# Performance work log

Hardware: AMD Instinct MI355X
Metric: run time of the kernel (lower is better)

## Reference

```python
import jax, jax.numpy as jnp
import numpy as np

HEAD_DIM = 64
FEAT_DIM = 64
WINDOW = 64
EPS = 1e-6


def _performer_phi(x, proj):
    # x: [..., D] float32, proj: [F, D]  ->  [..., F]
    scaled = x / (HEAD_DIM ** 0.25)
    projected = jnp.einsum('...d,fd->...f', scaled, proj)
    sq_norm = 0.5 * jnp.sum(scaled * scaled, axis=-1, keepdims=True)
    logits = jnp.clip(projected - sq_norm, -20.0, 20.0)
    return jnp.exp(logits) / np.sqrt(float(FEAT_DIM))


def setup_inputs() -> dict:
    key = jax.random.key(0)
    kq, kk, kv, kp = jax.random.split(key, 4)
    B, H, Hkv, T, D = 2, 32, 8, 4096, HEAD_DIM
    q = jax.random.normal(kq, (B, H, T, D), dtype=jnp.float32)
    k = jax.random.normal(kk, (B, Hkv, T, D), dtype=jnp.float32)
    v = jax.random.normal(kv, (B, Hkv, T, D), dtype=jnp.float32)
    # performer projection: orthogonal block, row-normalized (as in _build_projection_matrix)
    g = np.asarray(jax.random.normal(kp, (D, D), dtype=jnp.float32))
    qm, _ = np.linalg.qr(g)
    mat = qm[:, :FEAT_DIM].T  # [F, D]
    mat = mat / np.maximum(np.linalg.norm(mat, axis=-1, keepdims=True), 1e-6)
    proj = jnp.asarray(mat, dtype=jnp.float32)
    return {'q': q, 'k': k, 'v': v, 'proj': proj}


def reference(q, k, v, proj):
    # Hybrid attention: exact local-window softmax (current + previous block,
    # causal) fused with linear (Performer) attention over all fully-evicted
    # blocks via a recurrent SSD state, sharing a single normalizer.
    B, H, T, D = q.shape
    Hkv = k.shape[1]
    G = H // Hkv  # query heads per kv group (query_to_kv = arange(H) // G)
    W = WINDOW
    nb = T // W
    f32 = jnp.float32

    phi_q = _performer_phi(q.astype(f32), proj.astype(f32))  # [B,H,T,F]
    phi_k = _performer_phi(k.astype(f32), proj.astype(f32))  # [B,Hkv,T,F]

    pq = phi_q.reshape(B, Hkv, G, nb, W, FEAT_DIM)
    pk = phi_k.reshape(B, Hkv, nb, W, FEAT_DIM)
    qb = q.astype(f32).reshape(B, Hkv, G, nb, W, D)
    kb = k.astype(f32).reshape(B, Hkv, nb, W, D)
    vb = v.astype(f32).reshape(B, Hkv, nb, W, D)

    # ---- linear-attention recurrent state (state_decay = 1.0 -> plain cumsum)
    # state at query block c covers all blocks <= c-2 (blocks fully outside the
    # local window).
    S_blk = jnp.einsum('bknwf,bknwd->bknfd', pk, vb)  # [B,Hkv,nb,F,D]
    z_blk = pk.sum(axis=3)                            # [B,Hkv,nb,F]
    S_cum = jnp.cumsum(S_blk, axis=2)
    z_cum = jnp.cumsum(z_blk, axis=2)
    S_used = jnp.concatenate([jnp.zeros_like(S_cum[:, :, :2]), S_cum[:, :, :-2]], axis=2)
    z_used = jnp.concatenate([jnp.zeros_like(z_cum[:, :, :2]), z_cum[:, :, :-2]], axis=2)

    num_lin = jnp.einsum('bkgnwf,bknfd->bkgnwd', pq, S_used)  # [B,Hkv,G,nb,W,D]
    den_lin = jnp.einsum('bkgnwf,bknf->bkgnw', pq, z_used)    # [B,Hkv,G,nb,W]

    # ---- local softmax attention over [previous block | current block]
    k_prev = jnp.concatenate([jnp.zeros_like(kb[:, :, :1]), kb[:, :, :-1]], axis=2)
    v_prev = jnp.concatenate([jnp.zeros_like(vb[:, :, :1]), vb[:, :, :-1]], axis=2)
    kk2 = jnp.concatenate([k_prev, kb], axis=3)  # [B,Hkv,nb,2W,D]
    vv2 = jnp.concatenate([v_prev, vb], axis=3)

    scores = jnp.einsum('bkgnwd,bknxd->bkgnwx', qb, kk2) / np.sqrt(float(D))
    jj = jnp.arange(W)[:, None]        # query offset in block
    ii = jnp.arange(2 * W)[None, :]    # key offset in 2-block window
    causal = ii <= (W + jj)            # [W, 2W]
    has_prev = (jnp.arange(nb) > 0)[:, None, None]
    mask = causal[None] & (has_prev | (ii >= W)[None])  # [nb, W, 2W]
    a = jnp.where(mask[None, None, None], jnp.exp(jnp.clip(scores, -30.0, 30.0)), 0.0)

    num_loc = jnp.einsum('bkgnwx,bknxd->bkgnwd', a, vv2)
    den = a.sum(axis=-1) + den_lin + EPS  # shared normalizer

    out = (num_loc + num_lin) / den[..., None]
    return out.reshape(B, H, T, D).astype(q.dtype)
```

## Files before the change

### kernel.cpp

```cpp
#include <hip/hip_runtime.h>

#define BB 2
#define HKV 8
#define HH 32
#define TT 4096
#define NBLK 64
#define SCL 0.35355339059327373f
#define LOG2E 1.4426950408889634f

typedef __attribute__((ext_vector_type(8))) short short8;
typedef __attribute__((ext_vector_type(4))) float f32x4;
typedef unsigned int u32;

__device__ __forceinline__ unsigned short f2bf(float x) {
    union { float f; u32 u; } v; v.f = x;
    u32 r = v.u + 0x7fffu + ((v.u >> 16) & 1u);
    return (unsigned short)(r >> 16);
}
__device__ __forceinline__ u32 pk2(float lo, float hi) {
    u32 r;
    asm("v_cvt_pk_bf16_f32 %0, %1, %2" : "=v"(r) : "v"(lo), "v"(hi));
    return r;
}
__device__ __forceinline__ float bf2f(unsigned short b) {
    union { u32 u; float f; } v; v.u = ((u32)b) << 16; return v.f;
}
__device__ __forceinline__ f32x4 mfma16(short8 a, short8 b, f32x4 c) {
    return __builtin_amdgcn_mfma_f32_16x16x32_bf16(a, b, c, 0, 0, 0);
}
__device__ __forceinline__ short8 ldsfrag(const char* base, int row, int off) {
    int b = (row << 7) + off;
    b ^= (row & 7) << 4;
    return *(const short8*)(base + b);
}
__device__ __forceinline__ short8 xform(f32x4 t0, f32x4 t1, int lane) {
    const int c = lane & 15, g = lane >> 4;
    u32 p00 = pk2(t0[0], t0[1]), p01 = pk2(t0[2], t0[3]);
    u32 p10 = pk2(t1[0], t1[1]), p11 = pk2(t1[2], t1[3]);
    int srcA = c + 32 * (g & 1);
    int srcB = srcA + 16;
    u32 a00 = (u32)__shfl((int)p00, srcA);
    u32 a01 = (u32)__shfl((int)p01, srcA);
    u32 a10 = (u32)__shfl((int)p10, srcA);
    u32 a11 = (u32)__shfl((int)p11, srcA);
    u32 b00 = (u32)__shfl((int)p00, srcB);
    u32 b01 = (u32)__shfl((int)p01, srcB);
    u32 b10 = (u32)__shfl((int)p10, srcB);
    u32 b11 = (u32)__shfl((int)p11, srcB);
    bool hi = (g & 2);
    union { u32 u[4]; short8 s; } r;
    r.u[0] = hi ? a10 : a00;
    r.u[1] = hi ? a11 : a01;
    r.u[2] = hi ? b10 : b00;
    r.u[3] = hi ? b11 : b01;
    return r.s;
}
__device__ __forceinline__ void gld16(const void* g, void* l) {
    __builtin_amdgcn_global_load_lds((const __attribute__((address_space(1))) u32*)g,
                                     (__attribute__((address_space(3))) u32*)l, 16, 0, 0);
}

__global__ __launch_bounds__(256, 4) void k_phase1(
        const float* __restrict__ kg, const float* __restrict__ vg,
        const float* __restrict__ pg,
        char* __restrict__ sblk, char* __restrict__ kbf, char* __restrict__ vbf,
        float* __restrict__ zg) {
    __shared__ __align__(16) char kb_s[8192];
    __shared__ __align__(16) char vt_s[8192];
    __shared__ float sqn_s[64];

    const int tid = threadIdx.x;
    const int bid = blockIdx.x;
    const size_t base = (size_t)bid * 4096;

#pragma unroll
    for (int j = 0; j < 4; ++j) {
        int i4 = tid + j * 256;
        int key = i4 >> 4, d0 = (i4 & 15) << 2;
        float4 fk = *(const float4*)(kg + base + key * 64 + d0);
        float s0 = fk.x * SCL, s1 = fk.y * SCL, s2 = fk.z * SCL, s3 = fk.w * SCL;
        int byte = (key << 7) + (d0 << 1); byte ^= (key & 7) << 4;
        *(uint2*)(kb_s + byte) = make_uint2(pk2(s0, s1), pk2(s2, s3));
        float ps = 0.5f * (s0 * s0 + s1 * s1 + s2 * s2 + s3 * s3);
        ps += __shfl_xor(ps, 1);
        ps += __shfl_xor(ps, 2);
        ps += __shfl_xor(ps, 4);
        ps += __shfl_xor(ps, 8);
        if ((tid & 15) == 0) sqn_s[key] = ps;
    }
    {
        int d = tid & 63, kq = tid >> 6;
        const float* vp = vg + base + (size_t)kq * 16 * 64 + d;
        union { unsigned short h[16]; uint4 q[2]; } pk;
#pragma unroll
        for (int i = 0; i < 16; ++i) pk.h[i] = f2bf(vp[i * 64]);
        int b0 = ((d << 7) + (kq << 5)) ^ ((d & 7) << 4);
        int b1 = ((d << 7) + (kq << 5) + 16) ^ ((d & 7) << 4);
        *(uint4*)(vt_s + b0) = pk.q[0];
        *(uint4*)(vt_s + b1) = pk.q[1];
    }
    __syncthreads();

    {
        int off = tid * 16;
        *(float4*)(kbf + (size_t)bid * 8192 + off) = *(const float4*)(kb_s + off);
        *(float4*)(kbf + (size_t)bid * 8192 + off + 4096) = *(const float4*)(kb_s + off + 4096);
        *(float4*)(vbf + (size_t)bid * 8192 + off) = *(const float4*)(vt_s + off);
        *(float4*)(vbf + (size_t)bid * 8192 + off + 4096) = *(const float4*)(vt_s + off + 4096);
    }

    const int lane = tid & 63, wv = tid >> 6;
    const int c = lane & 15, g = lane >> 4;
    const int fb = wv * 16;

    const float* prow = pg + (size_t)(fb + c) * 64;
    short8 pjb[2];
#pragma unroll
    for (int kt = 0; kt < 2; ++kt) {
        int d0 = kt * 32 + g * 8;
        float4 f0 = *(const float4*)(prow + d0);
        float4 f1 = *(const float4*)(prow + d0 + 4);
        union { u32 u[4]; short8 s; } r;
        r.u[0] = pk2(f0.x, f0.y); r.u[1] = pk2(f0.z, f0.w);
        r.u[2] = pk2(f1.x, f1.y); r.u[3] = pk2(f1.z, f1.w);
        pjb[kt] = r.s;
    }

    f32x4 pc[4];
    float zp = 0.f;
#pragma unroll
    for (int t = 0; t < 4; ++t) {
        f32x4 s = {0.f, 0.f, 0.f, 0.f};
        s = mfma16(ldsfrag(kb_s, t * 16 + c, g * 16), pjb[0], s);
        s = mfma16(ldsfrag(kb_s, t * 16 + c, g * 16 + 64), pjb[1], s);
#pragma unroll
        for (int r = 0; r < 4; ++r) {
            int w = t * 16 + g * 4 + r;
            float p = exp2f(fmaf(s[r] - sqn_s[w], LOG2E, -3.0f));
            s[r] = p;
            zp += p;
        }
        pc[t] = s;
    }
    zp += __shfl_xor(zp, 16);
    zp += __shfl_xor(zp, 32);
    if (lane < 16) zg[(size_t)bid * 64 + fb + c] = zp;

    short8 pb0 = xform(pc[0], pc[1], lane);
    short8 pb1 = xform(pc[2], pc[3], lane);

    char* so = sblk + (size_t)bid * 8192;
#pragma unroll
    for (int dt = 0; dt < 4; ++dt) {
        f32x4 s = {0.f, 0.f, 0.f, 0.f};
        s = mfma16(ldsfrag(vt_s, dt * 16 + c, g * 16), pb0, s);
        s = mfma16(ldsfrag(vt_s, dt * 16 + c, g * 16 + 64), pb1, s);
#pragma unroll
        for (int r = 0; r < 4; ++r) {
            int d = dt * 16 + g * 4 + r;
            int byte = ((d << 7) + ((fb + c) << 1)) ^ ((d & 7) << 4);
            *(unsigned short*)(so + byte) = f2bf(s[r]);
        }
    }
}

__global__ __launch_bounds__(256) void k_scan(char* __restrict__ sblk,
                                              float* __restrict__ zg,
                                              const float* __restrict__ pg,
                                              char* __restrict__ pbf) {
    const int tid = threadIdx.x;
    const int bx = blockIdx.x;
    if (bx < 128) {
        int pair = bx >> 3;
        int u = ((bx & 7) << 8) + tid;
        char* p = sblk + (size_t)pair * 64 * 8192 + (size_t)u * 4;
        float c0a = 0.f, c1a = 0.f, c0b = 0.f, c1b = 0.f;
        for (int n8 = 0; n8 < 64; n8 += 8) {
            u32 w[8];
#pragma unroll
            for (int j = 0; j < 8; ++j)
                w[j] = *(const u32*)(p + (size_t)(n8 + j) * 8192);
#pragma unroll
            for (int j = 0; j < 8; ++j) {
                *(u32*)(p + (size_t)(n8 + j) * 8192) = pk2(c0a, c0b);
                float va = bf2f((unsigned short)(w[j] & 0xffff));
                float vb = bf2f((unsigned short)(w[j] >> 16));
                c0a = c1a; c1a += va;
                c0b = c1b; c1b += vb;
            }
        }
    } else if (bx < 132) {
        int i = ((bx - 128) << 8) + tid;
        int pair = i >> 6, f = i & 63;
        float* zp = zg + (size_t)pair * 64 * 64 + f;
        float c0 = 0.f, c1 = 0.f;
        for (int n8 = 0; n8 < 64; n8 += 8) {
            float w[8];
#pragma unroll
            for (int j = 0; j < 8; ++j) w[j] = zp[(size_t)(n8 + j) * 64];
#pragma unroll
            for (int j = 0; j < 8; ++j) {
                zp[(size_t)(n8 + j) * 64] = c0;
                c0 = c1; c1 += w[j];
            }
        }
    } else {
#pragma unroll
        for (int j = 0; j < 4; ++j) {
            int i4 = tid + j * 256;
            int row = i4 >> 4, d0 = (i4 & 15) << 2;
            float4 f = *(const float4*)(pg + row * 64 + d0);
            int byte = ((row << 7) + (d0 << 1)) ^ ((row & 7) << 4);
            *(uint2*)(pbf + byte) = make_uint2(pk2(f.x, f.y), pk2(f.z, f.w));
        }
    }
}

__global__ __launch_bounds__(256, 3) void k_main(
        const float* __restrict__ qg,
        const char* __restrict__ kbf, const char* __restrict__ vbf,
        const char* __restrict__ sbf, const char* __restrict__ pbf,
        const float* __restrict__ zg, float* __restrict__ outg) {
    __shared__ __align__(16) char smem[24576];

    const int tid = threadIdx.x;
    const int orig = blockIdx.x;
    const int bid = (orig & 7) * 256 + (orig >> 3);
    const int pr = bid & 1;
    const int n = (bid >> 1) & 63;
    const int kv = (bid >> 7) & 7;
    const int b = bid >> 10;
    const int h0 = kv * 4 + pr * 2;
    const int iblk = ((b * HKV + kv) << 6) + n;
    const int lane = tid & 63, wv = tid >> 6;
    const int c = lane & 15, g = lane >> 4;
    const int qr = wv * 16 + c;
    const bool hasprev = (n > 0);

    const size_t qrow0A = (size_t)(b * HH + h0) * TT + (size_t)n * 64;
    const size_t qrow0B = qrow0A + TT;
    const float* qrowA = qg + (qrow0A + qr) * 64;
    const float* qrowB = qg + (qrow0B + qr) * 64;
    float4 qfA[4], qfB[4];
    qfA[0] = *(const float4*)(qrowA + g * 8);
    qfA[1] = *(const float4*)(qrowA + g * 8 + 4);
    qfA[2] = *(const float4*)(qrowA + 32 + g * 8);
    qfA[3] = *(const float4*)(qrowA + 32 + g * 8 + 4);
    qfB[0] = *(const float4*)(qrowB + g * 8);
    qfB[1] = *(const float4*)(qrowB + g * 8 + 4);
    qfB[2] = *(const float4*)(qrowB + 32 + g * 8);
    qfB[3] = *(const float4*)(qrowB + 32 + g * 8 + 4);

    {
        const char* gs[3] = {kbf + (size_t)(iblk - 1) * 8192, kbf + (size_t)iblk * 8192,
                             vbf + (size_t)iblk * 8192};
#pragma unroll
        for (int ci = 0; ci < 6; ++ci) {
            int cch = wv * 6 + ci;
            int seg = cch >> 3, off = (cch & 7) << 10;
            if (n == 0 && seg == 0) continue;
            gld16(gs[seg] + off + lane * 16, smem + (seg << 13) + off);
        }
        if (n == 0) {
            uint4 zz = {0, 0, 0, 0};
            *(uint4*)(smem + tid * 32) = zz;
            *(uint4*)(smem + tid * 32 + 16) = zz;
        }
    }

    float4 zv[4];
#pragma unroll
    for (int ft = 0; ft < 4; ++ft)
        zv[ft] = *(const float4*)(zg + (size_t)iblk * 64 + ft * 16 + g * 4);

    float sqA = 0.f, sqB = 0.f;
    short8 qbA[2], qbB[2];
#pragma unroll
    for (int kt = 0; kt < 2; ++kt) {
        {
            float4 f0 = qfA[kt * 2], f1 = qfA[kt * 2 + 1];
            float s0 = f0.x * SCL, s1 = f0.y * SCL, s2 = f0.z * SCL, s3 = f0.w * SCL;
            float s4 = f1.x * SCL, s5 = f1.y * SCL, s6 = f1.z * SCL, s7 = f1.w * SCL;
            sqA += s0 * s0 + s1 * s1 + s2 * s2 + s3 * s3 + s4 * s4 + s5 * s5 + s6 * s6 + s7 * s7;
            union { u32 u[4]; short8 s; } r;
            r.u[0] = pk2(s0, s1); r.u[1] = pk2(s2, s3);
            r.u[2] = pk2(s4, s5); r.u[3] = pk2(s6, s7);
            qbA[kt] = r.s;
        }
        {
            float4 f0 = qfB[kt * 2], f1 = qfB[kt * 2 + 1];
            float s0 = f0.x * SCL, s1 = f0.y * SCL, s2 = f0.z * SCL, s3 = f0.w * SCL;
            float s4 = f1.x * SCL, s5 = f1.y * SCL, s6 = f1.z * SCL, s7 = f1.w * SCL;
            sqB += s0 * s0 + s1 * s1 + s2 * s2 + s3 * s3 + s4 * s4 + s5 * s5 + s6 * s6 + s7 * s7;
            union { u32 u[4]; short8 s; } r;
            r.u[0] = pk2(s0, s1); r.u[1] = pk2(s2, s3);
            r.u[2] = pk2(s4, s5); r.u[3] = pk2(s6, s7);
            qbB[kt] = r.s;
        }
    }
    sqA += __shfl_xor(sqA, 16);
    sqA += __shfl_xor(sqA, 32);
    sqB += __shfl_xor(sqB, 16);
    sqB += __shfl_xor(sqB, 32);
    const float sqnA = 0.5f * sqA, sqnB = 0.5f * sqB;

    __syncthreads();

    const char* K2 = smem;
    const char* VTP = smem;
    const char* VTC = smem + 16384;

    short8 abA[4], abB[4];
    float asumA = 0.f, asumB = 0.f;
#pragma unroll
    for (int p = 0; p < 4; ++p) {
        if (p == 2) {
            __syncthreads();
            if (hasprev) {
                const char* vp = vbf + (size_t)(iblk - 1) * 8192;
                gld16(vp + ((wv * 2 + 0) << 10) + lane * 16, smem + ((wv * 2 + 0) << 10));
                gld16(vp + ((wv * 2 + 1) << 10) + lane * 16, smem + ((wv * 2 + 1) << 10));
            }
        }
        f32x4 tA0, tA1, tB0, tB1;
#pragma unroll
        for (int half = 0; half < 2; ++half) {
            int t = p * 2 + half;
            short8 ka0 = ldsfrag(K2, t * 16 + c, g * 16);
            short8 ka1 = ldsfrag(K2, t * 16 + c, g * 16 + 64);
            f32x4 scA = {0.f, 0.f, 0.f, 0.f};
            scA = mfma16(ka0, qbA[0], scA);
            scA = mfma16(ka1, qbA[1], scA);
            f32x4 scB = {0.f, 0.f, 0.f, 0.f};
            scB = mfma16(ka0, qbB[0], scB);
            scB = mfma16(ka1, qbB[1], scB);
#pragma unroll
            for (int r = 0; r < 4; ++r) {
                int key = t * 16 + g * 4 + r;
                bool valid = (key >= 64) ? ((key - 64) <= qr) : hasprev;
                float aA = valid ? __expf(scA[r]) : 0.f;
                float aB = valid ? __expf(scB[r]) : 0.f;
                scA[r] = aA; asumA += aA;
                scB[r] = aB; asumB += aB;
            }
            if (half == 0) { tA0 = scA; tB0 = scB; } else { tA1 = scA; tB1 = scB; }
        }
        abA[p] = xform(tA0, tA1, lane);
        abB[p] = xform(tB0, tB1, lane);
    }
    asumA += __shfl_xor(asumA, 16);
    asumA += __shfl_xor(asumA, 32);
    asumB += __shfl_xor(asumB, 16);
    asumB += __shfl_xor(asumB, 32);

    float dlA = 0.f, dlB = 0.f;
    short8 pbA[2], pbB[2];
#pragma unroll
    for (int pp = 0; pp < 2; ++pp) {
        f32x4 uA0, uA1, uB0, uB1;
#pragma unroll
        for (int half = 0; half < 2; ++half) {
            int ft = pp * 2 + half;
            short8 pj0 = ldsfrag(pbf, ft * 16 + c, g * 16);
            short8 pj1 = ldsfrag(pbf, ft * 16 + c, g * 16 + 64);
            f32x4 pfA = {0.f, 0.f, 0.f, 0.f};
            pfA = mfma16(pj0, qbA[0], pfA);
            pfA = mfma16(pj1, qbA[1], pfA);
            f32x4 pfB = {0.f, 0.f, 0.f, 0.f};
            pfB = mfma16(pj0, qbB[0], pfB);
            pfB = mfma16(pj1, qbB[1], pfB);
#pragma unroll
            for (int r = 0; r < 4; ++r) {
                float zr = ((const float*)&zv[ft])[r];
                float pvA = exp2f(fmaf(pfA[r] - sqnA, LOG2E, -3.0f));
                float pvB = exp2f(fmaf(pfB[r] - sqnB, LOG2E, -3.0f));
                pfA[r] = pvA; dlA += pvA * zr;
                pfB[r] = pvB; dlB += pvB * zr;
            }
            if (half == 0) { uA0 = pfA; uB0 = pfB; } else { uA1 = pfA; uB1 = pfB; }
        }
        pbA[pp] = xform(uA0, uA1, lane);
        pbB[pp] = xform(uB0, uB1, lane);
    }
    dlA += __shfl_xor(dlA, 16);
    dlA += __shfl_xor(dlA, 32);
    dlB += __shfl_xor(dlB, 16);
    dlB += __shfl_xor(dlB, 32);

    __syncthreads();

    const char* stp = sbf + (size_t)iblk * 8192;
    const float invA = 1.f / (asumA + dlA + 1e-6f);
    const float invB = 1.f / (asumB + dlB + 1e-6f);
    float* orowA = outg + (qrow0A + qr) * 64;
    float* orowB = outg + (qrow0B + qr) * 64;
#pragma unroll
    for (int dt = 0; dt < 4; ++dt) {
        short8 vp0 = ldsfrag(VTP, dt * 16 + c, g * 16);
        short8 vp1 = ldsfrag(VTP, dt * 16 + c, g * 16 + 64);
        short8 vc0 = ldsfrag(VTC, dt * 16 + c, g * 16);
        short8 vc1 = ldsfrag(VTC, dt * 16 + c, g * 16 + 64);
        short8 st0 = ldsfrag(stp, dt * 16 + c, g * 16);
        short8 st1 = ldsfrag(stp, dt * 16 + c, g * 16 + 64);
        f32x4 aA = {0.f, 0.f, 0.f, 0.f};
        aA = mfma16(vp0, abA[0], aA);
        aA = mfma16(vp1, abA[1], aA);
        aA = mfma16(vc0, abA[2], aA);
        aA = mfma16(vc1, abA[3], aA);
        aA = mfma16(st0, pbA[0], aA);
        aA = mfma16(st1, pbA[1], aA);
        f32x4 aB = {0.f, 0.f, 0.f, 0.f};
        aB = mfma16(vp0, abB[0], aB);
        aB = mfma16(vp1, abB[1], aB);
        aB = mfma16(vc0, abB[2], aB);
        aB = mfma16(vc1, abB[3], aB);
        aB = mfma16(st0, pbB[0], aB);
        aB = mfma16(st1, pbB[1], aB);
#pragma unroll
        for (int r = 0; r < 4; ++r) {
            orowA[dt * 16 + g * 4 + r] = aA[r] * invA;
            orowB[dt * 16 + g * 4 + r] = aB[r] * invB;
        }
    }
}

extern "C" void kernel_launch(void* const* d_in, const int* in_sizes, int n_in,
                              void* d_out, int out_size, void* d_ws, size_t ws_size,
                              hipStream_t stream) {
    const float* q = (const float*)d_in[0];
    const float* k = (const float*)d_in[1];
    const float* v = (const float*)d_in[2];
    const float* proj = (const float*)d_in[3];
    float* out = (float*)d_out;

    char* ws = (char*)d_ws;
    char* sblk = ws;
    char* kbf = ws + (8u << 20);
    char* vbf = ws + (16u << 20);
    float* z = (float*)(ws + (24u << 20));
    char* pbf = ws + (24u << 20) + (256u << 10);

    k_phase1<<<dim3(1024), dim3(256), 0, stream>>>(k, v, proj, sblk, kbf, vbf, z);
    k_scan<<<dim3(133), dim3(256), 0, stream>>>(sblk, z, proj, pbf);
    k_main<<<dim3(2048), dim3(256), 0, stream>>>(q, kbf, vbf, sblk, pbf, z, out);
}
```

Before: 58.61 us.

## Prefetch previous V block and state fragments upfront, drop mid-kernel barriers

```diff
diff --git a/kernel.cpp b/kernel.cpp
--- a/kernel.cpp
+++ b/kernel.cpp
@@ -221,7 +221,7 @@
         const char* __restrict__ kbf, const char* __restrict__ vbf,
         const char* __restrict__ sbf, const char* __restrict__ pbf,
         const float* __restrict__ zg, float* __restrict__ outg) {
-    __shared__ __align__(16) char smem[24576];
+    __shared__ __align__(16) char smem[32768];
 
     const int tid = threadIdx.x;
     const int orig = blockIdx.x;
@@ -252,20 +252,28 @@
     qfB[3] = *(const float4*)(qrowB + 32 + g * 8 + 4);
 
     {
-        const char* gs[3] = {kbf + (size_t)(iblk - 1) * 8192, kbf + (size_t)iblk * 8192,
-                             vbf + (size_t)iblk * 8192};
-#pragma unroll
-        for (int ci = 0; ci < 6; ++ci) {
-            int cch = wv * 6 + ci;
+        const char* gs[4] = {kbf + (size_t)(iblk - 1) * 8192, kbf + (size_t)iblk * 8192,
+                             vbf + (size_t)(iblk - 1) * 8192, vbf + (size_t)iblk * 8192};
+#pragma unroll
+        for (int ci = 0; ci < 8; ++ci) {
+            int cch = wv * 8 + ci;
             int seg = cch >> 3, off = (cch & 7) << 10;
-            if (n == 0 && seg == 0) continue;
+            if (n == 0 && (seg == 0 || seg == 2)) continue;
             gld16(gs[seg] + off + lane * 16, smem + (seg << 13) + off);
         }
         if (n == 0) {
             uint4 zz = {0, 0, 0, 0};
-            *(uint4*)(smem + tid * 32) = zz;
-            *(uint4*)(smem + tid * 32 + 16) = zz;
-        }
+            *(uint4*)(smem + 16384 + tid * 32) = zz;
+            *(uint4*)(smem + 16384 + tid * 32 + 16) = zz;
+        }
+    }
+
+    const char* stp = sbf + (size_t)iblk * 8192;
+    short8 st[8];
+#pragma unroll
+    for (int dt = 0; dt < 4; ++dt) {
+        st[dt * 2 + 0] = ldsfrag(stp, dt * 16 + c, g * 16);
+        st[dt * 2 + 1] = ldsfrag(stp, dt * 16 + c, g * 16 + 64);
     }
 
     float4 zv[4];
@@ -307,21 +315,13 @@
     __syncthreads();
 
     const char* K2 = smem;
-    const char* VTP = smem;
-    const char* VTC = smem + 16384;
+    const char* VTP = smem + 16384;
+    const char* VTC = smem + 24576;
 
     short8 abA[4], abB[4];
     float asumA = 0.f, asumB = 0.f;
 #pragma unroll
     for (int p = 0; p < 4; ++p) {
-        if (p == 2) {
-            __syncthreads();
-            if (hasprev) {
-                const char* vp = vbf + (size_t)(iblk - 1) * 8192;
-                gld16(vp + ((wv * 2 + 0) << 10) + lane * 16, smem + ((wv * 2 + 0) << 10));
-                gld16(vp + ((wv * 2 + 1) << 10) + lane * 16, smem + ((wv * 2 + 1) << 10));
-            }
-        }
         f32x4 tA0, tA1, tB0, tB1;
 #pragma unroll
         for (int half = 0; half < 2; ++half) {
@@ -387,9 +387,6 @@
     dlB += __shfl_xor(dlB, 16);
     dlB += __shfl_xor(dlB, 32);
 
-    __syncthreads();
-
-    const char* stp = sbf + (size_t)iblk * 8192;
     const float invA = 1.f / (asumA + dlA + 1e-6f);
     const float invB = 1.f / (asumB + dlB + 1e-6f);
     float* orowA = outg + (qrow0A + qr) * 64;
@@ -400,22 +397,20 @@
         short8 vp1 = ldsfrag(VTP, dt * 16 + c, g * 16 + 64);
         short8 vc0 = ldsfrag(VTC, dt * 16 + c, g * 16);
         short8 vc1 = ldsfrag(VTC, dt * 16 + c, g * 16 + 64);
-        short8 st0 = ldsfrag(stp, dt * 16 + c, g * 16);
-        short8 st1 = ldsfrag(stp, dt * 16 + c, g * 16 + 64);
         f32x4 aA = {0.f, 0.f, 0.f, 0.f};
         aA = mfma16(vp0, abA[0], aA);
         aA = mfma16(vp1, abA[1], aA);
         aA = mfma16(vc0, abA[2], aA);
         aA = mfma16(vc1, abA[3], aA);
-        aA = mfma16(st0, pbA[0], aA);
-        aA = mfma16(st1, pbA[1], aA);
+        aA = mfma16(st[dt * 2 + 0], pbA[0], aA);
+        aA = mfma16(st[dt * 2 + 1], pbA[1], aA);
         f32x4 aB = {0.f, 0.f, 0.f, 0.f};
         aB = mfma16(vp0, abB[0], aB);
         aB = mfma16(vp1, abB[1], aB);
         aB = mfma16(vc0, abB[2], aB);
         aB = mfma16(vc1, abB[3], aB);
-        aB = mfma16(st0, pbB[0], aB);
-        aB = mfma16(st1, pbB[1], aB);
+        aB = mfma16(st[dt * 2 + 0], pbB[0], aB);
+        aB = mfma16(st[dt * 2 + 1], pbB[1], aB);
 #pragma unroll
         for (int r = 0; r < 4; ++r) {
             orowA[dt * 16 + g * 4 + r] = aA[r] * invA;
```

Result: slower. 78.68 us (+34.2%).
